# Optimization experiments

Measured on AMD Instinct MI355X. Metric: run time of the kernel, lower is better.

Reference implementation:

```python
import jax, jax.numpy as jnp
import numpy as np

D_MODEL = 512
N_STATE = 512  # must equal D_MODEL (torch code broadcasts B*(N,) against u[:,t] of (batch,d_model))
BATCH = 8
SEQ_LEN = 4096
DT_MIN, DT_MAX = 0.001, 0.1


def setup_inputs() -> dict:
    key = jax.random.key(0)
    k_u, k_lam, k_b, k_q, k_dt = jax.random.split(key, 5)
    u = jax.random.normal(k_u, (BATCH, SEQ_LEN, D_MODEL), dtype=jnp.float32)
    Lambda = jax.random.normal(k_lam, (N_STATE,), dtype=jnp.float32)
    B = jax.random.normal(k_b, (N_STATE,), dtype=jnp.float32)
    Q = jax.random.normal(k_q, (N_STATE, D_MODEL), dtype=jnp.float32) / np.sqrt(N_STATE)
    log_dt = jax.random.uniform(k_dt, (1,), dtype=jnp.float32) * (np.log(DT_MAX) - np.log(DT_MIN)) + np.log(DT_MIN)
    return {"u": u, "Lambda": Lambda, "B": B, "Q": Q, "log_dt": log_dt}


def reference(u, Lambda, B, Q, log_dt):
    # dt = exp(log_dt); A = diag(exp(dt * -exp(Lambda))) -> x @ A.T == x * a
    dt = jnp.exp(log_dt)              # (1,)
    a = jnp.exp(dt * (-jnp.exp(Lambda)))  # (N,)
    Bdt = dt * B                      # (N,)

    u_t = jnp.transpose(u, (1, 0, 2))  # (L, batch, N)

    def step(x, ut):
        x = x * a + Bdt * ut           # diagonal recurrence, (batch, N)
        return x, x

    x0 = jnp.zeros((u.shape[0], Lambda.shape[0]), dtype=u.dtype)
    _, xs = jax.lax.scan(step, x0, u_t)       # (L, batch, N)
    y = jnp.einsum('lbn,nd->bld', xs, Q)      # project to d_model
    return y
```

## Files before the change

### kernel.cpp

```cpp
#include <hip/hip_runtime.h>
#include <hip/hip_bf16.h>

#define BATCH 8
#define SEQ   4096
#define NST   512
#define DM    512
#define NCHUNK 32
#define TCH    128
#define ST     64
#define LDP    (NST + 8)

typedef __attribute__((ext_vector_type(4))) float f32x4;
typedef __attribute__((ext_vector_type(2))) float f32x2;
typedef __attribute__((ext_vector_type(8))) short short8v;
typedef __attribute__((ext_vector_type(4))) short short4v;

__device__ __forceinline__ short f2bf(float f) {
  union { float f; unsigned u; } v; v.f = f;
  unsigned r = v.u + 0x7FFFu + ((v.u >> 16) & 1u);
  return (short)(r >> 16);
}

__global__ void k_scan_sums(const float* __restrict__ u, const float* __restrict__ Lam,
                            const float* __restrict__ Bv, const float* __restrict__ log_dt,
                            float* __restrict__ S) {
  int gid = blockIdx.x * 256 + threadIdx.x;
  int n2 = (gid & 255) * 2;
  int bc = gid >> 8;
  int b  = bc & (BATCH - 1);
  int c  = bc >> 3;
  float dt = expf(log_dt[0]);
  f32x2 lam = *(const f32x2*)(Lam + n2);
  f32x2 bv  = *(const f32x2*)(Bv + n2);
  float a0 = expf(-dt * expf(lam[0])), a1 = expf(-dt * expf(lam[1]));
  float g0 = dt * bv[0],               g1 = dt * bv[1];
  const float* up = u + ((size_t)b * SEQ + (size_t)c * TCH) * NST + n2;
  float s0 = 0.f, s1 = 0.f;
  #pragma unroll 8
  for (int t = 0; t < TCH; ++t) {
    f32x2 v = *(const f32x2*)(up + (size_t)t * NST);
    s0 = fmaf(a0, s0, g0 * v[0]);
    s1 = fmaf(a1, s1, g1 * v[1]);
  }
  *(f32x2*)(S + (c * BATCH + b) * NST + n2) = (f32x2){s0, s1};
}

__global__ void k_propagate(const float* __restrict__ Lam, const float* __restrict__ log_dt,
                            const float* __restrict__ S, float* __restrict__ Xc) {
  int gid = blockIdx.x * 256 + threadIdx.x;
  int n = gid & (NST - 1);
  int b = gid >> 9;
  float dt = expf(log_dt[0]);
  float a  = expf(-dt * expf(Lam[n]));
  float aT = a;
  #pragma unroll
  for (int i = 0; i < 7; ++i) aT *= aT;
  float x = 0.f;
  for (int c = 0; c < NCHUNK; ++c) {
    Xc[(c * BATCH + b) * NST + n] = x;
    x = fmaf(aT, x, S[(c * BATCH + b) * NST + n]);
  }
}

__global__ void k_transQ(const float* __restrict__ Q, short* __restrict__ Qt) {
  __shared__ short tile[64][68];
  int bn = (blockIdx.x & 7) * 64;
  int bd = (blockIdx.x >> 3) * 64;
  int tc = threadIdx.x & 15;
  int tr = threadIdx.x >> 4;
  #pragma unroll
  for (int i = 0; i < 4; ++i) {
    int r = tr + i * 16;
    f32x4 v = *(const f32x4*)(Q + (size_t)(bn + r) * DM + bd + tc * 4);
    short4v h;
    h[0] = f2bf(v[0]); h[1] = f2bf(v[1]); h[2] = f2bf(v[2]); h[3] = f2bf(v[3]);
    *(short4v*)&tile[r][tc * 4] = h;
  }
  __syncthreads();
  #pragma unroll
  for (int i = 0; i < 4; ++i) {
    int r = tr + i * 16;
    short4v h;
    #pragma unroll
    for (int j = 0; j < 4; ++j) h[j] = tile[tc * 4 + j][r];
    *(short4v*)(Qt + (size_t)(bd + r) * NST + bn + tc * 4) = h;
  }
}

__global__ __launch_bounds__(512) void k_fused(
    const float* __restrict__ u, const float* __restrict__ Lam,
    const float* __restrict__ Bv, const float* __restrict__ log_dt,
    const float* __restrict__ Xc, const short* __restrict__ Qt,
    float* __restrict__ y) {
  __shared__ __align__(16) short X[2][ST][LDP];
  const int tid = threadIdx.x;
  const int b = blockIdx.x & (BATCH - 1);
  const int c = blockIdx.x >> 3;

  const float dt = expf(log_dt[0]);
  const float a  = expf(-dt * expf(Lam[tid]));
  const float g  = dt * Bv[tid];
  float x = Xc[(c * BATCH + b) * NST + tid];
  const float* up = u + ((size_t)b * SEQ + (size_t)c * TCH) * NST + tid;

  {
    float ur[ST];
    #pragma unroll
    for (int t = 0; t < ST; ++t) ur[t] = up[(size_t)t * NST];
    #pragma unroll
    for (int t = 0; t < ST; ++t) {
      x = fmaf(a, x, g * ur[t]);
      X[0][t][tid] = f2bf(x);
    }
  }
  __syncthreads();

  const int lane = tid & 63;
  const int wc   = tid >> 6;
  const int l15  = lane & 15;
  const int lhi  = lane >> 4;
  const int ka   = lhi * 8;
  const short* qbase = Qt + (size_t)(wc * 64 + l15) * NST + ka;
  float* yb = y + ((size_t)b * SEQ + (size_t)c * TCH) * DM;

  float ur2[ST];
  f32x4 acc[4][4];
  #pragma unroll
  for (int mi = 0; mi < 4; ++mi)
    #pragma unroll
    for (int nf = 0; nf < 4; ++nf) acc[mi][nf] = (f32x4){0.f, 0.f, 0.f, 0.f};

  #pragma unroll
  for (int kk = 0; kk < 16; ++kk) {
    const int k0 = kk * 32;
    #pragma unroll
    for (int j = 0; j < 4; ++j)
      ur2[kk * 4 + j] = up[(size_t)(ST + kk * 4 + j) * NST];
    short8v afrag[4];
    #pragma unroll
    for (int mi = 0; mi < 4; ++mi)
      afrag[mi] = *(const short8v*)&X[0][mi * 16 + l15][k0 + ka];
    short8v bfrag[4];
    #pragma unroll
    for (int nf = 0; nf < 4; ++nf)
      bfrag[nf] = *(const short8v*)(qbase + (size_t)nf * 16 * NST + k0);
    #pragma unroll
    for (int mi = 0; mi < 4; ++mi)
      #pragma unroll
      for (int nf = 0; nf < 4; ++nf)
        acc[mi][nf] = __builtin_amdgcn_mfma_f32_16x16x32_bf16(afrag[mi], bfrag[nf], acc[mi][nf], 0, 0, 0);
  }

  #pragma unroll
  for (int mi = 0; mi < 4; ++mi)
    #pragma unroll
    for (int nf = 0; nf < 4; ++nf) {
      const int rr = mi * 16 + lhi * 4;
      const int cc = wc * 64 + nf * 16 + l15;
      #pragma unroll
      for (int i = 0; i < 4; ++i)
        yb[(size_t)(rr + i) * DM + cc] = acc[mi][nf][i];
    }

  #pragma unroll
  for (int t = 0; t < ST; ++t) {
    x = fmaf(a, x, g * ur2[t]);
    X[1][t][tid] = f2bf(x);
  }
  __syncthreads();

  #pragma unroll
  for (int mi = 0; mi < 4; ++mi)
    #pragma unroll
    for (int nf = 0; nf < 4; ++nf) acc[mi][nf] = (f32x4){0.f, 0.f, 0.f, 0.f};

  #pragma unroll
  for (int kk = 0; kk < 16; ++kk) {
    const int k0 = kk * 32;
    short8v afrag[4];
    #pragma unroll
    for (int mi = 0; mi < 4; ++mi)
      afrag[mi] = *(const short8v*)&X[1][mi * 16 + l15][k0 + ka];
    short8v bfrag[4];
    #pragma unroll
    for (int nf = 0; nf < 4; ++nf)
      bfrag[nf] = *(const short8v*)(qbase + (size_t)nf * 16 * NST + k0);
    #pragma unroll
    for (int mi = 0; mi < 4; ++mi)
      #pragma unroll
      for (int nf = 0; nf < 4; ++nf)
        acc[mi][nf] = __builtin_amdgcn_mfma_f32_16x16x32_bf16(afrag[mi], bfrag[nf], acc[mi][nf], 0, 0, 0);
  }

  #pragma unroll
  for (int mi = 0; mi < 4; ++mi)
    #pragma unroll
    for (int nf = 0; nf < 4; ++nf) {
      const int rr = ST + mi * 16 + lhi * 4;
      const int cc = wc * 64 + nf * 16 + l15;
      #pragma unroll
      for (int i = 0; i < 4; ++i)
        yb[(size_t)(rr + i) * DM + cc] = acc[mi][nf][i];
    }
}

extern "C" void kernel_launch(void* const* d_in, const int* in_sizes, int n_in,
                              void* d_out, int out_size, void* d_ws, size_t ws_size,
                              hipStream_t stream) {
  const float* u      = (const float*)d_in[0];
  const float* Lam    = (const float*)d_in[1];
  const float* Bv     = (const float*)d_in[2];
  const float* Q      = (const float*)d_in[3];
  const float* log_dt = (const float*)d_in[4];
  float* out = (float*)d_out;

  float* S  = (float*)d_ws;
  float* Xc = S + NCHUNK * BATCH * NST;
  short* Qt = (short*)(Xc + NCHUNK * BATCH * NST);

  hipLaunchKernelGGL(k_scan_sums, dim3(NCHUNK * BATCH), dim3(256), 0, stream,
                     u, Lam, Bv, log_dt, S);
  hipLaunchKernelGGL(k_propagate, dim3(BATCH * NST / 256), dim3(256), 0, stream,
                     Lam, log_dt, S, Xc);
  hipLaunchKernelGGL(k_transQ, dim3(64), dim3(256), 0, stream, Q, Qt);
  hipLaunchKernelGGL(k_fused, dim3(NCHUNK * BATCH), dim3(512), 0, stream,
                     u, Lam, Bv, log_dt, Xc, Qt, out);
}
```

Measured before the change: 65.55 us.

## Fuse chunked scan, propagation and projection into one cooperative kernel

Replaces the four-kernel pipeline with a single cooperative kernel. Each block transposes its share of Q, scans its chunk once from zero while keeping the states in registers, publishes the chunk sum, waits at a grid barrier, and then computes its carry-in directly from the earlier chunk sums. It corrects the local states with powers of a and runs one 128-row MFMA GEMM. This removes the second read of u and three extra launches. The cost is a grid-wide sync, heavy register use (128 states plus 32 accumulators per thread), and a redundant per-block prefix over the earlier chunks. The old path stays as a fallback if the cooperative launch fails.

```diff
diff --git a/kernel.cpp b/kernel.cpp
--- a/kernel.cpp
+++ b/kernel.cpp
@@ -1,5 +1,8 @@
 #include <hip/hip_runtime.h>
 #include <hip/hip_bf16.h>
+#include <hip/hip_cooperative_groups.h>
+
+namespace cg = cooperative_groups;
 
 #define BATCH 8
 #define SEQ   4096
@@ -7,7 +10,6 @@
 #define DM    512
 #define NCHUNK 32
 #define TCH    128
-#define ST     64
 #define LDP    (NST + 8)
 
 typedef __attribute__((ext_vector_type(4))) float f32x4;
@@ -19,6 +21,130 @@
   union { float f; unsigned u; } v; v.f = f;
   unsigned r = v.u + 0x7FFFu + ((v.u >> 16) & 1u);
   return (short)(r >> 16);
+}
+
+__global__ __launch_bounds__(512) void k_mega(
+    const float* __restrict__ u, const float* __restrict__ Lam,
+    const float* __restrict__ Bv, const float* __restrict__ log_dt,
+    const float* __restrict__ Q, float* __restrict__ S,
+    short* __restrict__ Qt, float* __restrict__ y) {
+  __shared__ __align__(16) short X[TCH][LDP];
+  const int tid = threadIdx.x;
+  const int b = blockIdx.x & (BATCH - 1);
+  const int c = blockIdx.x >> 3;
+
+  if (blockIdx.x < 64) {
+    short (*tile)[68] = (short(*)[68])&X[0][0];
+    const int bn = (blockIdx.x & 7) * 64;
+    const int bd = (blockIdx.x >> 3) * 64;
+    const int tc4 = (tid & 15) * 4;
+    const int tr = tid >> 4;
+    #pragma unroll
+    for (int i = 0; i < 2; ++i) {
+      int r = tr + i * 32;
+      f32x4 v = *(const f32x4*)(Q + (size_t)(bn + r) * DM + bd + tc4);
+      short4v h;
+      h[0] = f2bf(v[0]); h[1] = f2bf(v[1]); h[2] = f2bf(v[2]); h[3] = f2bf(v[3]);
+      *(short4v*)&tile[r][tc4] = h;
+    }
+    __syncthreads();
+    #pragma unroll
+    for (int i = 0; i < 2; ++i) {
+      int r = tr + i * 32;
+      short4v h;
+      #pragma unroll
+      for (int j = 0; j < 4; ++j) h[j] = tile[tc4 + j][r];
+      *(short4v*)(Qt + (size_t)(bd + r) * NST + bn + tc4) = h;
+    }
+    __syncthreads();
+  }
+
+  const float dt = expf(log_dt[0]);
+  const float a  = expf(-dt * expf(Lam[tid]));
+  const float g  = dt * Bv[tid];
+  const float* up = u + ((size_t)b * SEQ + (size_t)c * TCH) * NST + tid;
+  float xl[TCH];
+  {
+    float x = 0.f;
+    for (int t0 = 0; t0 < TCH; t0 += 32) {
+      float ur[32];
+      #pragma unroll
+      for (int j = 0; j < 32; ++j) ur[j] = up[(size_t)(t0 + j) * NST];
+      #pragma unroll
+      for (int j = 0; j < 32; ++j) { x = fmaf(a, x, g * ur[j]); xl[t0 + j] = x; }
+    }
+    S[(c * BATCH + b) * NST + tid] = x;
+  }
+  __threadfence();
+  cg::this_grid().sync();
+
+  float aT = a;
+  #pragma unroll
+  for (int i = 0; i < 7; ++i) aT *= aT;
+  float xin = 0.f;
+  {
+    int cp = 0;
+    for (; cp + 8 <= c; cp += 8) {
+      float sb[8];
+      #pragma unroll
+      for (int j = 0; j < 8; ++j) sb[j] = S[((cp + j) * BATCH + b) * NST + tid];
+      #pragma unroll
+      for (int j = 0; j < 8; ++j) xin = fmaf(aT, xin, sb[j]);
+    }
+    for (; cp < c; ++cp) xin = fmaf(aT, xin, S[(cp * BATCH + b) * NST + tid]);
+  }
+
+  {
+    float ap = a;
+    #pragma unroll
+    for (int t = 0; t < TCH; ++t) {
+      X[t][tid] = f2bf(fmaf(ap, xin, xl[t]));
+      ap *= a;
+    }
+  }
+  __syncthreads();
+
+  const int lane = tid & 63;
+  const int wc   = tid >> 6;
+  const int l15  = lane & 15;
+  const int lhi  = lane >> 4;
+  const int ka   = lhi * 8;
+  const short* qbase = Qt + (size_t)(wc * 64 + l15) * NST + ka;
+  float* yb = y + ((size_t)b * SEQ + (size_t)c * TCH) * DM;
+
+  f32x4 acc[8][4];
+  #pragma unroll
+  for (int mi = 0; mi < 8; ++mi)
+    #pragma unroll
+    for (int nf = 0; nf < 4; ++nf) acc[mi][nf] = (f32x4){0.f, 0.f, 0.f, 0.f};
+
+  for (int kk = 0; kk < 16; ++kk) {
+    const int k0 = kk * 32;
+    short8v bfrag[4];
+    #pragma unroll
+    for (int nf = 0; nf < 4; ++nf)
+      bfrag[nf] = *(const short8v*)(qbase + (size_t)nf * 16 * NST + k0);
+    short8v afrag[8];
+    #pragma unroll
+    for (int mi = 0; mi < 8; ++mi)
+      afrag[mi] = *(const short8v*)&X[mi * 16 + l15][k0 + ka];
+    #pragma unroll
+    for (int mi = 0; mi < 8; ++mi)
+      #pragma unroll
+      for (int nf = 0; nf < 4; ++nf)
+        acc[mi][nf] = __builtin_amdgcn_mfma_f32_16x16x32_bf16(afrag[mi], bfrag[nf], acc[mi][nf], 0, 0, 0);
+  }
+
+  #pragma unroll
+  for (int mi = 0; mi < 8; ++mi)
+    #pragma unroll
+    for (int nf = 0; nf < 4; ++nf) {
+      const int rr = mi * 16 + lhi * 4;
+      const int cc = wc * 64 + nf * 16 + l15;
+      #pragma unroll
+      for (int i = 0; i < 4; ++i)
+        yb[(size_t)(rr + i) * DM + cc] = acc[mi][nf][i];
+    }
 }
 
 __global__ void k_scan_sums(const float* __restrict__ u, const float* __restrict__ Lam,
@@ -92,29 +218,23 @@
     const float* __restrict__ Bv, const float* __restrict__ log_dt,
     const float* __restrict__ Xc, const short* __restrict__ Qt,
     float* __restrict__ y) {
-  __shared__ __align__(16) short X[2][ST][LDP];
+  __shared__ __align__(16) short X[2][64][LDP];
   const int tid = threadIdx.x;
   const int b = blockIdx.x & (BATCH - 1);
   const int c = blockIdx.x >> 3;
-
   const float dt = expf(log_dt[0]);
   const float a  = expf(-dt * expf(Lam[tid]));
   const float g  = dt * Bv[tid];
   float x = Xc[(c * BATCH + b) * NST + tid];
   const float* up = u + ((size_t)b * SEQ + (size_t)c * TCH) * NST + tid;
-
   {
-    float ur[ST];
-    #pragma unroll
-    for (int t = 0; t < ST; ++t) ur[t] = up[(size_t)t * NST];
-    #pragma unroll
-    for (int t = 0; t < ST; ++t) {
-      x = fmaf(a, x, g * ur[t]);
-      X[0][t][tid] = f2bf(x);
-    }
+    float ur[64];
+    #pragma unroll
+    for (int t = 0; t < 64; ++t) ur[t] = up[(size_t)t * NST];
+    #pragma unroll
+    for (int t = 0; t < 64; ++t) { x = fmaf(a, x, g * ur[t]); X[0][t][tid] = f2bf(x); }
   }
   __syncthreads();
-
   const int lane = tid & 63;
   const int wc   = tid >> 6;
   const int l15  = lane & 15;
@@ -122,35 +242,29 @@
   const int ka   = lhi * 8;
   const short* qbase = Qt + (size_t)(wc * 64 + l15) * NST + ka;
   float* yb = y + ((size_t)b * SEQ + (size_t)c * TCH) * DM;
-
-  float ur2[ST];
+  float ur2[64];
   f32x4 acc[4][4];
   #pragma unroll
   for (int mi = 0; mi < 4; ++mi)
     #pragma unroll
     for (int nf = 0; nf < 4; ++nf) acc[mi][nf] = (f32x4){0.f, 0.f, 0.f, 0.f};
-
   #pragma unroll
   for (int kk = 0; kk < 16; ++kk) {
     const int k0 = kk * 32;
     #pragma unroll
-    for (int j = 0; j < 4; ++j)
-      ur2[kk * 4 + j] = up[(size_t)(ST + kk * 4 + j) * NST];
+    for (int j = 0; j < 4; ++j) ur2[kk * 4 + j] = up[(size_t)(64 + kk * 4 + j) * NST];
     short8v afrag[4];
     #pragma unroll
-    for (int mi = 0; mi < 4; ++mi)
-      afrag[mi] = *(const short8v*)&X[0][mi * 16 + l15][k0 + ka];
+    for (int mi = 0; mi < 4; ++mi) afrag[mi] = *(const short8v*)&X[0][mi * 16 + l15][k0 + ka];
     short8v bfrag[4];
     #pragma unroll
-    for (int nf = 0; nf < 4; ++nf)
-      bfrag[nf] = *(const short8v*)(qbase + (size_t)nf * 16 * NST + k0);
+    for (int nf = 0; nf < 4; ++nf) bfrag[nf] = *(const short8v*)(qbase + (size_t)nf * 16 * NST + k0);
     #pragma unroll
     for (int mi = 0; mi < 4; ++mi)
       #pragma unroll
       for (int nf = 0; nf < 4; ++nf)
         acc[mi][nf] = __builtin_amdgcn_mfma_f32_16x16x32_bf16(afrag[mi], bfrag[nf], acc[mi][nf], 0, 0, 0);
   }
-
   #pragma unroll
   for (int mi = 0; mi < 4; ++mi)
     #pragma unroll
@@ -158,49 +272,38 @@
       const int rr = mi * 16 + lhi * 4;
       const int cc = wc * 64 + nf * 16 + l15;
       #pragma unroll
-      for (int i = 0; i < 4; ++i)
-        yb[(size_t)(rr + i) * DM + cc] = acc[mi][nf][i];
-    }
-
-  #pragma unroll
-  for (int t = 0; t < ST; ++t) {
-    x = fmaf(a, x, g * ur2[t]);
-    X[1][t][tid] = f2bf(x);
-  }
+      for (int i = 0; i < 4; ++i) yb[(size_t)(rr + i) * DM + cc] = acc[mi][nf][i];
+    }
+  #pragma unroll
+  for (int t = 0; t < 64; ++t) { x = fmaf(a, x, g * ur2[t]); X[1][t][tid] = f2bf(x); }
   __syncthreads();
-
   #pragma unroll
   for (int mi = 0; mi < 4; ++mi)
     #pragma unroll
     for (int nf = 0; nf < 4; ++nf) acc[mi][nf] = (f32x4){0.f, 0.f, 0.f, 0.f};
-
   #pragma unroll
   for (int kk = 0; kk < 16; ++kk) {
     const int k0 = kk * 32;
     short8v afrag[4];
     #pragma unroll
-    for (int mi = 0; mi < 4; ++mi)
-      afrag[mi] = *(const short8v*)&X[1][mi * 16 + l15][k0 + ka];
+    for (int mi = 0; mi < 4; ++mi) afrag[mi] = *(const short8v*)&X[1][mi * 16 + l15][k0 + ka];
     short8v bfrag[4];
     #pragma unroll
-    for (int nf = 0; nf < 4; ++nf)
-      bfrag[nf] = *(const short8v*)(qbase + (size_t)nf * 16 * NST + k0);
+    for (int nf = 0; nf < 4; ++nf) bfrag[nf] = *(const short8v*)(qbase + (size_t)nf * 16 * NST + k0);
     #pragma unroll
     for (int mi = 0; mi < 4; ++mi)
       #pragma unroll
       for (int nf = 0; nf < 4; ++nf)
         acc[mi][nf] = __builtin_amdgcn_mfma_f32_16x16x32_bf16(afrag[mi], bfrag[nf], acc[mi][nf], 0, 0, 0);
   }
-
   #pragma unroll
   for (int mi = 0; mi < 4; ++mi)
     #pragma unroll
     for (int nf = 0; nf < 4; ++nf) {
-      const int rr = ST + mi * 16 + lhi * 4;
+      const int rr = 64 + mi * 16 + lhi * 4;
       const int cc = wc * 64 + nf * 16 + l15;
       #pragma unroll
-      for (int i = 0; i < 4; ++i)
-        yb[(size_t)(rr + i) * DM + cc] = acc[mi][nf][i];
+      for (int i = 0; i < 4; ++i) yb[(size_t)(rr + i) * DM + cc] = acc[mi][nf][i];
     }
 }
 
@@ -218,11 +321,18 @@
   float* Xc = S + NCHUNK * BATCH * NST;
   short* Qt = (short*)(Xc + NCHUNK * BATCH * NST);
 
-  hipLaunchKernelGGL(k_scan_sums, dim3(NCHUNK * BATCH), dim3(256), 0, stream,
-                     u, Lam, Bv, log_dt, S);
-  hipLaunchKernelGGL(k_propagate, dim3(BATCH * NST / 256), dim3(256), 0, stream,
-                     Lam, log_dt, S, Xc);
-  hipLaunchKernelGGL(k_transQ, dim3(64), dim3(256), 0, stream, Q, Qt);
-  hipLaunchKernelGGL(k_fused, dim3(NCHUNK * BATCH), dim3(512), 0, stream,
-                     u, Lam, Bv, log_dt, Xc, Qt, out);
-}
+  void* args[] = {(void*)&u, (void*)&Lam, (void*)&Bv, (void*)&log_dt,
+                  (void*)&Q, (void*)&S, (void*)&Qt, (void*)&out};
+  hipError_t e = hipLaunchCooperativeKernel((const void*)k_mega,
+                                            dim3(NCHUNK * BATCH), dim3(512),
+                                            args, 0, stream);
+  if (e != hipSuccess) {
+    hipLaunchKernelGGL(k_scan_sums, dim3(NCHUNK * BATCH), dim3(256), 0, stream,
+                       u, Lam, Bv, log_dt, S);
+    hipLaunchKernelGGL(k_propagate, dim3(BATCH * NST / 256), dim3(256), 0, stream,
+                       Lam, log_dt, S, Xc);
+    hipLaunchKernelGGL(k_transQ, dim3(64), dim3(256), 0, stream, Q, Qt);
+    hipLaunchKernelGGL(k_fused, dim3(NCHUNK * BATCH), dim3(512), 0, stream,
+                       u, Lam, Bv, log_dt, Xc, Qt, out);
+  }
+}
```

New measurement: 139.0 us. 2.12x slower.

## Halve chunk length to double fused-kernel blocks and drop in-block sub-chunk pipeline

Applied to the files above, without the earlier changes.

Sequence chunks shrink from 128 to 64 steps, so the chunk-sum, propagate and fused kernels get twice as many chunks and the fused kernel launches 512 blocks instead of 256. Each fused block now runs one scan-plus-MFMA pass over 64 timesteps with a single LDS buffer, removing the second sub-chunk and its overlapped prefetch of u. The aim is better CU occupancy and less LDS and register pressure per block. In exchange the carry-propagation kernel does twice as many serial steps, the Q fragments are reloaded by twice as many blocks, and the MFMA loop is only partly unrolled. The Q transpose kernel is also moved to launch first.

```diff
diff --git a/kernel.cpp b/kernel.cpp
--- a/kernel.cpp
+++ b/kernel.cpp
@@ -5,9 +5,8 @@
 #define SEQ   4096
 #define NST   512
 #define DM    512
-#define NCHUNK 32
-#define TCH    128
-#define ST     64
+#define NCHUNK 64
+#define TCH    64
 #define LDP    (NST + 8)
 
 typedef __attribute__((ext_vector_type(4))) float f32x4;
@@ -54,7 +53,7 @@
   float a  = expf(-dt * expf(Lam[n]));
   float aT = a;
   #pragma unroll
-  for (int i = 0; i < 7; ++i) aT *= aT;
+  for (int i = 0; i < 6; ++i) aT *= aT;
   float x = 0.f;
   for (int c = 0; c < NCHUNK; ++c) {
     Xc[(c * BATCH + b) * NST + n] = x;
@@ -92,25 +91,24 @@
     const float* __restrict__ Bv, const float* __restrict__ log_dt,
     const float* __restrict__ Xc, const short* __restrict__ Qt,
     float* __restrict__ y) {
-  __shared__ __align__(16) short X[2][ST][LDP];
+  __shared__ __align__(16) short X[TCH][LDP];
   const int tid = threadIdx.x;
   const int b = blockIdx.x & (BATCH - 1);
   const int c = blockIdx.x >> 3;
 
-  const float dt = expf(log_dt[0]);
-  const float a  = expf(-dt * expf(Lam[tid]));
-  const float g  = dt * Bv[tid];
-  float x = Xc[(c * BATCH + b) * NST + tid];
-  const float* up = u + ((size_t)b * SEQ + (size_t)c * TCH) * NST + tid;
-
   {
-    float ur[ST];
+    const float dt = expf(log_dt[0]);
+    const float a  = expf(-dt * expf(Lam[tid]));
+    const float g  = dt * Bv[tid];
+    float x  = Xc[(c * BATCH + b) * NST + tid];
+    const float* up = u + ((size_t)b * SEQ + (size_t)c * TCH) * NST + tid;
+    float ur[TCH];
     #pragma unroll
-    for (int t = 0; t < ST; ++t) ur[t] = up[(size_t)t * NST];
+    for (int t = 0; t < TCH; ++t) ur[t] = up[(size_t)t * NST];
     #pragma unroll
-    for (int t = 0; t < ST; ++t) {
+    for (int t = 0; t < TCH; ++t) {
       x = fmaf(a, x, g * ur[t]);
-      X[0][t][tid] = f2bf(x);
+      X[t][tid] = f2bf(x);
     }
   }
   __syncthreads();
@@ -123,23 +121,19 @@
   const short* qbase = Qt + (size_t)(wc * 64 + l15) * NST + ka;
   float* yb = y + ((size_t)b * SEQ + (size_t)c * TCH) * DM;
 
-  float ur2[ST];
   f32x4 acc[4][4];
   #pragma unroll
   for (int mi = 0; mi < 4; ++mi)
     #pragma unroll
     for (int nf = 0; nf < 4; ++nf) acc[mi][nf] = (f32x4){0.f, 0.f, 0.f, 0.f};
 
-  #pragma unroll
+  #pragma unroll 4
   for (int kk = 0; kk < 16; ++kk) {
     const int k0 = kk * 32;
-    #pragma unroll
-    for (int j = 0; j < 4; ++j)
-      ur2[kk * 4 + j] = up[(size_t)(ST + kk * 4 + j) * NST];
     short8v afrag[4];
     #pragma unroll
     for (int mi = 0; mi < 4; ++mi)
-      afrag[mi] = *(const short8v*)&X[0][mi * 16 + l15][k0 + ka];
+      afrag[mi] = *(const short8v*)&X[mi * 16 + l15][k0 + ka];
     short8v bfrag[4];
     #pragma unroll
     for (int nf = 0; nf < 4; ++nf)
@@ -161,47 +155,6 @@
       for (int i = 0; i < 4; ++i)
         yb[(size_t)(rr + i) * DM + cc] = acc[mi][nf][i];
     }
-
-  #pragma unroll
-  for (int t = 0; t < ST; ++t) {
-    x = fmaf(a, x, g * ur2[t]);
-    X[1][t][tid] = f2bf(x);
-  }
-  __syncthreads();
-
-  #pragma unroll
-  for (int mi = 0; mi < 4; ++mi)
-    #pragma unroll
-    for (int nf = 0; nf < 4; ++nf) acc[mi][nf] = (f32x4){0.f, 0.f, 0.f, 0.f};
-
-  #pragma unroll
-  for (int kk = 0; kk < 16; ++kk) {
-    const int k0 = kk * 32;
-    short8v afrag[4];
-    #pragma unroll
-    for (int mi = 0; mi < 4; ++mi)
-      afrag[mi] = *(const short8v*)&X[1][mi * 16 + l15][k0 + ka];
-    short8v bfrag[4];
-    #pragma unroll
-    for (int nf = 0; nf < 4; ++nf)
-      bfrag[nf] = *(const short8v*)(qbase + (size_t)nf * 16 * NST + k0);
-    #pragma unroll
-    for (int mi = 0; mi < 4; ++mi)
-      #pragma unroll
-      for (int nf = 0; nf < 4; ++nf)
-        acc[mi][nf] = __builtin_amdgcn_mfma_f32_16x16x32_bf16(afrag[mi], bfrag[nf], acc[mi][nf], 0, 0, 0);
-  }
-
-  #pragma unroll
-  for (int mi = 0; mi < 4; ++mi)
-    #pragma unroll
-    for (int nf = 0; nf < 4; ++nf) {
-      const int rr = ST + mi * 16 + lhi * 4;
-      const int cc = wc * 64 + nf * 16 + l15;
-      #pragma unroll
-      for (int i = 0; i < 4; ++i)
-        yb[(size_t)(rr + i) * DM + cc] = acc[mi][nf][i];
-    }
 }
 
 extern "C" void kernel_launch(void* const* d_in, const int* in_sizes, int n_in,
@@ -218,11 +171,11 @@
   float* Xc = S + NCHUNK * BATCH * NST;
   short* Qt = (short*)(Xc + NCHUNK * BATCH * NST);
 
+  hipLaunchKernelGGL(k_transQ, dim3(64), dim3(256), 0, stream, Q, Qt);
   hipLaunchKernelGGL(k_scan_sums, dim3(NCHUNK * BATCH), dim3(256), 0, stream,
                      u, Lam, Bv, log_dt, S);
   hipLaunchKernelGGL(k_propagate, dim3(BATCH * NST / 256), dim3(256), 0, stream,
                      Lam, log_dt, S, Xc);
-  hipLaunchKernelGGL(k_transQ, dim3(64), dim3(256), 0, stream, Q, Qt);
   hipLaunchKernelGGL(k_fused, dim3(NCHUNK * BATCH), dim3(512), 0, stream,
                      u, Lam, Bv, log_dt, Xc, Qt, out);
 }
```

Result: slower. 69.97 us (+6.7%).
